# Kernel tuning notes

Hardware: AMD Instinct MI355X
Metric: run time of the kernel (lower is better)

## Reference

```python
import jax, jax.numpy as jnp
import numpy as np

HEADS = 8
DIM_HEAD = 64
SCALE = DIM_HEAD ** -0.5  # q scaling
EPS = 1e-5  # channel LayerNorm eps (float32)


def setup_inputs() -> dict:
    key = jax.random.key(0)
    ks = jax.random.split(key, 4)
    B, C, H, W = 8, 256, 64, 64
    hd = HEADS * DIM_HEAD  # 512
    x = jax.random.normal(ks[0], (B, C, H, W), dtype=jnp.float32)
    w_qkv = jax.random.normal(ks[1], (3 * hd, C), dtype=jnp.float32) * 0.02  # 1x1 conv, no bias
    w_out = jax.random.normal(ks[2], (C, hd), dtype=jnp.float32) * 0.02     # 1x1 conv
    b_out = jax.random.normal(ks[3], (C,), dtype=jnp.float32) * 0.02
    g_ln = jnp.ones((C,), dtype=jnp.float32)  # LayerNorm gamma
    return {"x": x, "w_qkv": w_qkv, "w_out": w_out, "b_out": b_out, "g_ln": g_ln}


def reference(x, w_qkv, w_out, b_out, g_ln):
    B, C, H, W = x.shape
    n = H * W
    hd = HEADS * DIM_HEAD
    # 1x1 conv == per-pixel matmul: [B,C,H,W] x [3hd,C] -> [B,3hd,H,W]
    qkv = jnp.einsum('bchw,oc->bohw', x, w_qkv).reshape(B, 3, HEADS, DIM_HEAD, n)
    q, k, v = qkv[:, 0], qkv[:, 1], qkv[:, 2]  # each [B,h,d,n]
    q = jax.nn.softmax(q, axis=-2) * SCALE      # softmax over head-dim d
    k = jax.nn.softmax(k, axis=-1)              # softmax over spatial n
    v = v / n
    context = jnp.einsum('bhdn,bhen->bhde', k, v)   # [B,h,d,e]
    out = jnp.einsum('bhde,bhdn->bhen', context, q)  # [B,h,e,n]
    out = out.reshape(B, hd, H, W)
    # to_out: 1x1 conv + bias, then channel-wise LayerNorm (gamma only)
    y = jnp.einsum('bchw,oc->bohw', out, w_out) + b_out[None, :, None, None]
    mean = jnp.mean(y, axis=1, keepdims=True)
    var = jnp.var(y, axis=1, keepdims=True)  # unbiased=False
    return (y - mean) * jax.lax.rsqrt(var + EPS) * g_ln[None, :, None, None]
```

## Files before the change

### kernel.cpp

```cpp
#include <hip/hip_runtime.h>
#include <stdint.h>


#define NB    8
#define CCH   256
#define NSP   4096
#define O3    1536
#define NH    8
#define DH    64
#define CSTR  136

typedef unsigned short u16;
typedef unsigned int   u32;
typedef __bf16 bf16;
typedef bf16  bf16x8 __attribute__((ext_vector_type(8)));
typedef float f32x4  __attribute__((ext_vector_type(4)));
typedef u16   u16x8  __attribute__((ext_vector_type(8)));
typedef u16   u16x4  __attribute__((ext_vector_type(4)));

__device__ __forceinline__ float b2f(u16 h) {
  union { u32 u; float f; } x; x.u = ((u32)h) << 16; return x.f;
}
__device__ __forceinline__ u16 f2b(float f) {
  union { float f; u32 u; } x; x.f = f;
  u32 r = x.u + 0x7fffu + ((x.u >> 16) & 1u);
  return (u16)(r >> 16);
}
__device__ __forceinline__ int detect_bf(const void* g) {
  return ((const u32*)g)[0] != 0x3F800000u;
}
__device__ __forceinline__ void ldg2lds16(const u16* g, u16* l) {
  __builtin_amdgcn_global_load_lds((const __attribute__((address_space(1))) void*)g,
                                   (__attribute__((address_space(3))) void*)l,
                                   16, 0, 0);
}

#define TSTR 68
__global__ __launch_bounds__(256) void k_prep(const void* __restrict__ xv,
                                              const void* __restrict__ wv,
                                              u16* __restrict__ xT,
                                              u16* __restrict__ Wb,
                                              float* __restrict__ S,
                                              const void* __restrict__ g_lnv) {
  const int isbf = detect_bf(g_lnv);
  const int t = threadIdx.x;
  if (blockIdx.z == 8) {
    const int tid = blockIdx.y * 64 + blockIdx.x;
    if (tid < 192) {
      const int idx = tid * 256 + t;
      const int row = idx >> 5, cu = idx & 31;
      int nr;
      if (row < 512)       nr = row;
      else if (row < 1024) nr = 512 + ((row - 512) >> 6) * 128 + (row & 63);
      else                 nr = 512 + ((row - 1024) >> 6) * 128 + 64 + (row & 63);
      const int didx = nr * 32 + cu;
      if (isbf) {
        reinterpret_cast<uint4*>(Wb)[didx] = reinterpret_cast<const uint4*>(wv)[idx];
      } else {
        float4 a = reinterpret_cast<const float4*>(wv)[idx * 2];
        float4 b = reinterpret_cast<const float4*>(wv)[idx * 2 + 1];
        ushort4 o0, o1;
        o0.x = f2b(a.x); o0.y = f2b(a.y); o0.z = f2b(a.z); o0.w = f2b(a.w);
        o1.x = f2b(b.x); o1.y = f2b(b.y); o1.z = f2b(b.z); o1.w = f2b(b.w);
        reinterpret_cast<ushort4*>(Wb)[didx * 2]     = o0;
        reinterpret_cast<ushort4*>(Wb)[didx * 2 + 1] = o1;
      }
    } else if (tid < 200) {
      reinterpret_cast<float2*>(S)[(tid - 192) * 256 + t] = (float2){0.f, 0.f};
    }
    return;
  }
  const int b = blockIdx.z, cb = blockIdx.y * 64, nb = blockIdx.x * 64;
  __shared__ u16 tile[64 * TSTR];
  if (isbf) {
    const u16* xb = (const u16*)xv;
#pragma unroll
    for (int rr = 0; rr < 2; ++rr) {
      const int u = t + 256 * rr;
      const int c = u >> 3, ch = u & 7;
      u16x8 v = *reinterpret_cast<const u16x8*>(
          xb + ((size_t)(b * CCH + cb + c) * NSP + nb + ch * 8));
      u16* dst = tile + c * TSTR + ch * 8;
      *reinterpret_cast<u16x4*>(dst)     = (u16x4){v[0], v[1], v[2], v[3]};
      *reinterpret_cast<u16x4*>(dst + 4) = (u16x4){v[4], v[5], v[6], v[7]};
    }
  } else {
    const float* xb = (const float*)xv;
#pragma unroll
    for (int rr = 0; rr < 4; ++rr) {
      const int u = t + 256 * rr;
      const int c = u >> 4, c4 = u & 15;
      float4 f = *reinterpret_cast<const float4*>(
          xb + ((size_t)(b * CCH + cb + c) * NSP + nb + c4 * 4));
      u16x4 o; o[0] = f2b(f.x); o[1] = f2b(f.y); o[2] = f2b(f.z); o[3] = f2b(f.w);
      *reinterpret_cast<u16x4*>(tile + c * TSTR + c4 * 4) = o;
    }
  }
  __syncthreads();
#pragma unroll
  for (int rr = 0; rr < 2; ++rr) {
    const int u = t + 256 * rr;
    const int n = u >> 3, cc = u & 7;
    u16x8 o;
#pragma unroll
    for (int e = 0; e < 8; ++e) o[e] = tile[(cc * 8 + e) * TSTR + n];
    *reinterpret_cast<u16x8*>(
        xT + ((size_t)(b * NSP + nb + n) * CCH + cb + cc * 8)) = o;
  }
}

__global__ __launch_bounds__(256) void k_q_mfma(const u16* __restrict__ Wb,
                                                const u16* __restrict__ xT,
                                                u16* __restrict__ qT) {
  __shared__ __align__(16) u16 As[4096];
  __shared__ __align__(16) u16 Bs[4096];
  const int b = blockIdx.z, m0 = blockIdx.y * 128, n0 = blockIdx.x * 128;
  const int t = threadIdx.x, w = t >> 6, l = t & 63;
  const int wm = (w >> 1) * 64, wn = (w & 1) * 64;
  const int fr = l & 15, quad = l >> 4;

  f32x4 acc[4][4];
#pragma unroll
  for (int i = 0; i < 4; ++i)
#pragma unroll
    for (int j = 0; j < 4; ++j) acc[i][j] = (f32x4){0.f, 0.f, 0.f, 0.f};

  {
    const u16* A = Wb;
    const u16* B = xT + (size_t)b * NSP * CCH;
    const int s0 = w * 2, s1 = s0 + 1;
    const int ra0 = s0 * 16 + (l >> 2);
    const int ra1 = s1 * 16 + (l >> 2);
    const int kc  = (l & 3) * 8;
    const int fq  = quad * 8;
    for (int k0 = 0; k0 < 256; k0 += 32) {
      ldg2lds16(A + (size_t)(m0 + ra0) * 256 + k0 + kc, As + s0 * 512);
      ldg2lds16(A + (size_t)(m0 + ra1) * 256 + k0 + kc, As + s1 * 512);
      ldg2lds16(B + (size_t)(n0 + ra0) * 256 + k0 + kc, Bs + s0 * 512);
      ldg2lds16(B + (size_t)(n0 + ra1) * 256 + k0 + kc, Bs + s1 * 512);
      asm volatile("s_waitcnt vmcnt(0)" ::: "memory");
      __syncthreads();
      bf16x8 af[4], bg[4];
#pragma unroll
      for (int i = 0; i < 4; ++i)
        af[i] = *reinterpret_cast<const bf16x8*>(As + (wm + i * 16 + fr) * 32 + fq);
#pragma unroll
      for (int j = 0; j < 4; ++j)
        bg[j] = *reinterpret_cast<const bf16x8*>(Bs + (wn + j * 16 + fr) * 32 + fq);
#pragma unroll
      for (int i = 0; i < 4; ++i)
#pragma unroll
        for (int j = 0; j < 4; ++j)
          acc[i][j] = __builtin_amdgcn_mfma_f32_16x16x32_bf16(af[i], bg[j], acc[i][j], 0, 0, 0);
      __syncthreads();
    }
  }

  const int h = (m0 >> 6) + (w >> 1);
  u16* qTb = qT + (size_t)b * NSP * 512 + h * 64;
#pragma unroll
  for (int j = 0; j < 4; ++j) {
    float s = 0.f;
#pragma unroll
    for (int i = 0; i < 4; ++i)
#pragma unroll
      for (int r = 0; r < 4; ++r) { acc[i][j][r] = __expf(acc[i][j][r]); s += acc[i][j][r]; }
    s += __shfl_xor(s, 16);
    s += __shfl_xor(s, 32);
    const float inv = 0.125f / s;
    const int n = n0 + wn + j * 16 + fr;
#pragma unroll
    for (int i = 0; i < 4; ++i) {
      ushort4 o;
      o.x = f2b(acc[i][j][0] * inv); o.y = f2b(acc[i][j][1] * inv);
      o.z = f2b(acc[i][j][2] * inv); o.w = f2b(acc[i][j][3] * inv);
      *reinterpret_cast<ushort4*>(qTb + (size_t)n * 512 + i * 16 + quad * 4) = o;
    }
  }
}

__global__ __launch_bounds__(256) void k_kv_mfma(const u16* __restrict__ Wb,
                                                 const u16* __restrict__ xT,
                                                 float* __restrict__ S,
                                                 float* __restrict__ ctxp) {
  __shared__ __align__(16) u16 pool[64 * CSTR * 2];
  u16* As = pool;
  u16* Bs = pool + 4096;
  u16* ekS = pool;
  u16* vS  = pool + 64 * CSTR;

  const int b = blockIdx.z, h = blockIdx.y, n0 = blockIdx.x * 128;
  const int m0 = 512 + h * 128;
  const int t = threadIdx.x, w = t >> 6, l = t & 63;
  const int wm = (w >> 1) * 64, wn = (w & 1) * 64;
  const int fr = l & 15, quad = l >> 4;

  f32x4 acc[4][4];
#pragma unroll
  for (int i = 0; i < 4; ++i)
#pragma unroll
    for (int j = 0; j < 4; ++j) acc[i][j] = (f32x4){0.f, 0.f, 0.f, 0.f};

  {
    const u16* A = Wb;
    const u16* B = xT + (size_t)b * NSP * CCH;
    const int s0 = w * 2, s1 = s0 + 1;
    const int ra0 = s0 * 16 + (l >> 2);
    const int ra1 = s1 * 16 + (l >> 2);
    const int kc  = (l & 3) * 8;
    const int fq  = quad * 8;
    for (int k0 = 0; k0 < 256; k0 += 32) {
      ldg2lds16(A + (size_t)(m0 + ra0) * 256 + k0 + kc, As + s0 * 512);
      ldg2lds16(A + (size_t)(m0 + ra1) * 256 + k0 + kc, As + s1 * 512);
      ldg2lds16(B + (size_t)(n0 + ra0) * 256 + k0 + kc, Bs + s0 * 512);
      ldg2lds16(B + (size_t)(n0 + ra1) * 256 + k0 + kc, Bs + s1 * 512);
      asm volatile("s_waitcnt vmcnt(0)" ::: "memory");
      __syncthreads();
      bf16x8 af[4], bg[4];
#pragma unroll
      for (int i = 0; i < 4; ++i)
        af[i] = *reinterpret_cast<const bf16x8*>(As + (wm + i * 16 + fr) * 32 + fq);
#pragma unroll
      for (int j = 0; j < 4; ++j)
        bg[j] = *reinterpret_cast<const bf16x8*>(Bs + (wn + j * 16 + fr) * 32 + fq);
#pragma unroll
      for (int i = 0; i < 4; ++i)
#pragma unroll
        for (int j = 0; j < 4; ++j)
          acc[i][j] = __builtin_amdgcn_mfma_f32_16x16x32_bf16(af[i], bg[j], acc[i][j], 0, 0, 0);
      __syncthreads();
    }
  }

  {
    u16* dstT = (w < 2) ? ekS : vS;
#pragma unroll
    for (int i = 0; i < 4; ++i)
#pragma unroll
      for (int r = 0; r < 4; ++r) {
        const int row = i * 16 + quad * 4 + r;
#pragma unroll
        for (int j = 0; j < 4; ++j) {
          float v = acc[i][j][r];
          if (w < 2) v = __expf(v);
          dstT[row * CSTR + wn + j * 16 + fr] = f2b(v);
        }
      }
  }
  __syncthreads();

  {
    const int d = t >> 2, seg = t & 3;
    float s = 0.f;
    const u16* src = ekS + d * CSTR + seg * 32;
#pragma unroll
    for (int m = 0; m < 32; ++m) s += b2f(src[m]);
    s += __shfl_xor(s, 1);
    s += __shfl_xor(s, 2);
    if ((t & 3) == 0) atomicAdd(&S[b * 512 + h * 64 + d], s);
  }

  f32x4 c2[4];
#pragma unroll
  for (int j = 0; j < 4; ++j) c2[j] = (f32x4){0.f, 0.f, 0.f, 0.f};
#pragma unroll
  for (int k0 = 0; k0 < 128; k0 += 32) {
    bf16x8 af = *reinterpret_cast<const bf16x8*>(ekS + (w * 16 + fr) * CSTR + k0 + quad * 8);
#pragma unroll
    for (int j = 0; j < 4; ++j) {
      bf16x8 bg = *reinterpret_cast<const bf16x8*>(vS + (j * 16 + fr) * CSTR + k0 + quad * 8);
      c2[j] = __builtin_amdgcn_mfma_f32_16x16x32_bf16(af, bg, c2[j], 0, 0, 0);
    }
  }
  float* cb = ctxp + ((size_t)blockIdx.x * 64 + b * NH + h) * 4096;
#pragma unroll
  for (int j = 0; j < 4; ++j)
#pragma unroll
    for (int r = 0; r < 4; ++r)
      cb[(w * 16 + quad * 4 + r) * 64 + j * 16 + fr] = c2[j][r];
}

__global__ __launch_bounds__(256) void k_fold(const float* __restrict__ ctxp,
                                              const void* __restrict__ w_outv,
                                              const float* __restrict__ S,
                                              u16* __restrict__ Mb,
                                              const void* __restrict__ g_lnv) {
  const int isbf = detect_bf(g_lnv);
  const int h = blockIdx.x, b = blockIdx.y, ds = blockIdx.z * 16;
  const int t = threadIdx.x;
  __shared__ float ctxS[16][64];
  __shared__ float invS[16];
  if (t < 16) invS[t] = (1.0f / 4096.0f) / S[b * 512 + h * 64 + ds + t];
  const size_t bhoff = (size_t)(b * NH + h) * 4096 + (size_t)ds * 64;
#pragma unroll
  for (int i = 0; i < 4; ++i) {
    const int idx = t + 256 * i;
    float s = 0.f;
#pragma unroll
    for (int ch = 0; ch < 32; ++ch)
      s += ctxp[(size_t)ch * 64 * 4096 + bhoff + idx];
    ctxS[idx >> 6][idx & 63] = s;
  }
  float wrow[64];
  if (isbf) {
    const u16* wsrc = (const u16*)w_outv + (size_t)t * 512 + h * DH;
#pragma unroll
    for (int e4 = 0; e4 < 64; e4 += 4) {
      ushort4 u = *reinterpret_cast<const ushort4*>(wsrc + e4);
      wrow[e4 + 0] = b2f(u.x); wrow[e4 + 1] = b2f(u.y);
      wrow[e4 + 2] = b2f(u.z); wrow[e4 + 3] = b2f(u.w);
    }
  } else {
    const float* wsrc = (const float*)w_outv + (size_t)t * 512 + h * DH;
#pragma unroll
    for (int e4 = 0; e4 < 64; e4 += 4) {
      float4 f = *reinterpret_cast<const float4*>(wsrc + e4);
      wrow[e4 + 0] = f.x; wrow[e4 + 1] = f.y;
      wrow[e4 + 2] = f.z; wrow[e4 + 3] = f.w;
    }
  }
  __syncthreads();
  u16* dst = Mb + ((size_t)(b * CCH + t)) * 512 + h * DH + ds;
  for (int d = 0; d < 16; ++d) {
    float s = 0.f;
#pragma unroll
    for (int e = 0; e < 64; e += 4) {
      float4 c4 = *reinterpret_cast<const float4*>(&ctxS[d][e]);
      s += wrow[e] * c4.x + wrow[e + 1] * c4.y + wrow[e + 2] * c4.z + wrow[e + 3] * c4.w;
    }
    dst[d] = f2b(s * invS[d]);
  }
}

__global__ __launch_bounds__(512) void k_mq_ln(const u16* __restrict__ Mb,
                                               const u16* __restrict__ qT,
                                               const void* __restrict__ b_outv,
                                               const void* __restrict__ g_lnv,
                                               void* __restrict__ outv) {
  __shared__ __align__(16) u16 As[256 * 32];
  __shared__ __align__(16) u16 Bs[64 * 32];
  __shared__ float redS[8][4][16];
  __shared__ float redQ[8][4][16];
  __shared__ float gS[256], bS[256];

  const int isbf = detect_bf(g_lnv);
  const int b  = blockIdx.y;
  const int n0 = blockIdx.x * 64;
  const int t  = threadIdx.x, w = t >> 6, l = t & 63;

  if (t < 256) {
    gS[t] = isbf ? b2f(((const u16*)g_lnv)[t]) : ((const float*)g_lnv)[t];
    bS[t] = isbf ? b2f(((const u16*)b_outv)[t]) : ((const float*)b_outv)[t];
  }

  f32x4 acc[2][4];
#pragma unroll
  for (int i = 0; i < 2; ++i)
#pragma unroll
    for (int j = 0; j < 4; ++j) acc[i][j] = (f32x4){0.f, 0.f, 0.f, 0.f};

  const u16* A = Mb + (size_t)b * CCH * 512;
  const u16* B = qT + (size_t)b * NSP * 512;
  const int lr = l >> 2, kc = (l & 3) * 8;
  const int fr = l & 15, fq = (l >> 4) * 8;
  const int quad = l >> 4;

  for (int k0 = 0; k0 < 512; k0 += 32) {
    ldg2lds16(A + (size_t)(w * 32 + lr) * 512 + k0 + kc, As + (2 * w) * 512);
    ldg2lds16(A + (size_t)(w * 32 + 16 + lr) * 512 + k0 + kc, As + (2 * w + 1) * 512);
    if (w < 4)
      ldg2lds16(B + (size_t)(n0 + w * 16 + lr) * 512 + k0 + kc, Bs + w * 512);
    asm volatile("s_waitcnt vmcnt(0)" ::: "memory");
    __syncthreads();
    bf16x8 af[2], bg[4];
#pragma unroll
    for (int i = 0; i < 2; ++i)
      af[i] = *reinterpret_cast<const bf16x8*>(As + (w * 32 + i * 16 + fr) * 32 + fq);
#pragma unroll
    for (int j = 0; j < 4; ++j)
      bg[j] = *reinterpret_cast<const bf16x8*>(Bs + (j * 16 + fr) * 32 + fq);
#pragma unroll
    for (int i = 0; i < 2; ++i)
#pragma unroll
      for (int j = 0; j < 4; ++j)
        acc[i][j] = __builtin_amdgcn_mfma_f32_16x16x32_bf16(af[i], bg[j], acc[i][j], 0, 0, 0);
    __syncthreads();
  }

  float ps[4] = {}, pq[4] = {};
#pragma unroll
  for (int i = 0; i < 2; ++i)
#pragma unroll
    for (int r = 0; r < 4; ++r) {
      const int c = w * 32 + i * 16 + quad * 4 + r;
      const float bi = bS[c];
#pragma unroll
      for (int j = 0; j < 4; ++j) {
        acc[i][j][r] += bi;
        ps[j] += acc[i][j][r];
        pq[j] += acc[i][j][r] * acc[i][j][r];
      }
    }
#pragma unroll
  for (int j = 0; j < 4; ++j) {
    ps[j] += __shfl_xor(ps[j], 16); ps[j] += __shfl_xor(ps[j], 32);
    pq[j] += __shfl_xor(pq[j], 16); pq[j] += __shfl_xor(pq[j], 32);
  }
  if (quad == 0) {
#pragma unroll
    for (int j = 0; j < 4; ++j) { redS[w][j][fr] = ps[j]; redQ[w][j][fr] = pq[j]; }
  }
  __syncthreads();
  float mean[4], inv[4];
#pragma unroll
  for (int j = 0; j < 4; ++j) {
    float s = 0.f, q = 0.f;
#pragma unroll
    for (int g = 0; g < 8; ++g) { s += redS[g][j][fr]; q += redQ[g][j][fr]; }
    const float mn = s * (1.0f / 256.0f);
    const float vr = q * (1.0f / 256.0f) - mn * mn;
    mean[j] = mn;
    inv[j] = rsqrtf(vr + 1e-5f);
  }

#pragma unroll
  for (int i = 0; i < 2; ++i)
#pragma unroll
    for (int r = 0; r < 4; ++r) {
      const int c = w * 32 + i * 16 + quad * 4 + r;
      const float g = gS[c];
#pragma unroll
      for (int j = 0; j < 4; ++j) {
        const int col = n0 + j * 16 + fr;
        const float o = (acc[i][j][r] - mean[j]) * inv[j] * g;
        const size_t idx = ((size_t)b * CCH + c) * NSP + col;
        if (isbf) ((u16*)outv)[idx] = f2b(o);
        else      ((float*)outv)[idx] = o;
      }
    }
}

extern "C" void kernel_launch(void* const* d_in, const int* in_sizes, int n_in,
                              void* d_out, int out_size, void* d_ws, size_t ws_size,
                              hipStream_t stream) {
  (void)in_sizes; (void)n_in; (void)out_size; (void)ws_size;
  const void* x     = d_in[0];
  const void* w_qkv = d_in[1];
  const void* w_out = d_in[2];
  const void* b_out = d_in[3];
  const void* g_ln  = d_in[4];

  char* ws = (char*)d_ws;
  u16*   Wb   = (u16*)(ws + 256);
  float* S    = (float*)(ws + 851968);
  u16*   xT   = (u16*)(ws + 1048576);
  u16*   qT   = (u16*)(ws + 17825792);
  float* ctxp = (float*)(ws + 51380224);
  u16*   Mb   = (u16*)(ws + 84934656);

  k_prep    <<<dim3(64, 4, 9),  256, 0, stream>>>(x, w_qkv, xT, Wb, S, g_ln);
  k_q_mfma  <<<dim3(32, 4, NB), 256, 0, stream>>>(Wb, xT, qT);
  k_kv_mfma <<<dim3(32, NH, NB),256, 0, stream>>>(Wb, xT, S, ctxp);
  k_fold    <<<dim3(NH, NB, 4), 256, 0, stream>>>(ctxp, w_out, S, Mb, g_ln);
  k_mq_ln   <<<dim3(64, NB),    512, 0, stream>>>(Mb, qT, b_out, g_ln, d_out);
}
```

Before: 173.5 us.

## Fuse q projection and softmax into final output GEMM via LDS

Removes the separate q-projection kernel and the global qT buffer. The final kernel now computes the q tile for its 64 pixels, applies the head-dim softmax, and stores it in a swizzled 64 KB LDS buffer, then runs the M·q GEMM reading q from LDS. The operands for both GEMMs are loaded straight from global into registers with no LDS staging or per-step barriers. This avoids a roughly 32 MB qT write and read-back plus one launch, but it cuts occupancy because of the large LDS footprint and relies on cache hits for the direct global loads.

```diff
diff --git a/kernel.cpp b/kernel.cpp
--- a/kernel.cpp
+++ b/kernel.cpp
@@ -109,12 +109,18 @@
   }
 }
 
-__global__ __launch_bounds__(256) void k_q_mfma(const u16* __restrict__ Wb,
-                                                const u16* __restrict__ xT,
-                                                u16* __restrict__ qT) {
-  __shared__ __align__(16) u16 As[4096];
-  __shared__ __align__(16) u16 Bs[4096];
-  const int b = blockIdx.z, m0 = blockIdx.y * 128, n0 = blockIdx.x * 128;
+__global__ __launch_bounds__(256) void k_kv_mfma(const u16* __restrict__ Wb,
+                                                 const u16* __restrict__ xT,
+                                                 float* __restrict__ S,
+                                                 float* __restrict__ ctxp) {
+  __shared__ __align__(16) u16 pool[64 * CSTR * 2];
+  u16* As = pool;
+  u16* Bs = pool + 4096;
+  u16* ekS = pool;
+  u16* vS  = pool + 64 * CSTR;
+
+  const int b = blockIdx.z, h = blockIdx.y, n0 = blockIdx.x * 128;
+  const int m0 = 512 + h * 128;
   const int t = threadIdx.x, w = t >> 6, l = t & 63;
   const int wm = (w >> 1) * 64, wn = (w & 1) * 64;
   const int fr = l & 15, quad = l >> 4;
@@ -156,82 +162,6 @@
     }
   }
 
-  const int h = (m0 >> 6) + (w >> 1);
-  u16* qTb = qT + (size_t)b * NSP * 512 + h * 64;
-#pragma unroll
-  for (int j = 0; j < 4; ++j) {
-    float s = 0.f;
-#pragma unroll
-    for (int i = 0; i < 4; ++i)
-#pragma unroll
-      for (int r = 0; r < 4; ++r) { acc[i][j][r] = __expf(acc[i][j][r]); s += acc[i][j][r]; }
-    s += __shfl_xor(s, 16);
-    s += __shfl_xor(s, 32);
-    const float inv = 0.125f / s;
-    const int n = n0 + wn + j * 16 + fr;
-#pragma unroll
-    for (int i = 0; i < 4; ++i) {
-      ushort4 o;
-      o.x = f2b(acc[i][j][0] * inv); o.y = f2b(acc[i][j][1] * inv);
-      o.z = f2b(acc[i][j][2] * inv); o.w = f2b(acc[i][j][3] * inv);
-      *reinterpret_cast<ushort4*>(qTb + (size_t)n * 512 + i * 16 + quad * 4) = o;
-    }
-  }
-}
-
-__global__ __launch_bounds__(256) void k_kv_mfma(const u16* __restrict__ Wb,
-                                                 const u16* __restrict__ xT,
-                                                 float* __restrict__ S,
-                                                 float* __restrict__ ctxp) {
-  __shared__ __align__(16) u16 pool[64 * CSTR * 2];
-  u16* As = pool;
-  u16* Bs = pool + 4096;
-  u16* ekS = pool;
-  u16* vS  = pool + 64 * CSTR;
-
-  const int b = blockIdx.z, h = blockIdx.y, n0 = blockIdx.x * 128;
-  const int m0 = 512 + h * 128;
-  const int t = threadIdx.x, w = t >> 6, l = t & 63;
-  const int wm = (w >> 1) * 64, wn = (w & 1) * 64;
-  const int fr = l & 15, quad = l >> 4;
-
-  f32x4 acc[4][4];
-#pragma unroll
-  for (int i = 0; i < 4; ++i)
-#pragma unroll
-    for (int j = 0; j < 4; ++j) acc[i][j] = (f32x4){0.f, 0.f, 0.f, 0.f};
-
-  {
-    const u16* A = Wb;
-    const u16* B = xT + (size_t)b * NSP * CCH;
-    const int s0 = w * 2, s1 = s0 + 1;
-    const int ra0 = s0 * 16 + (l >> 2);
-    const int ra1 = s1 * 16 + (l >> 2);
-    const int kc  = (l & 3) * 8;
-    const int fq  = quad * 8;
-    for (int k0 = 0; k0 < 256; k0 += 32) {
-      ldg2lds16(A + (size_t)(m0 + ra0) * 256 + k0 + kc, As + s0 * 512);
-      ldg2lds16(A + (size_t)(m0 + ra1) * 256 + k0 + kc, As + s1 * 512);
-      ldg2lds16(B + (size_t)(n0 + ra0) * 256 + k0 + kc, Bs + s0 * 512);
-      ldg2lds16(B + (size_t)(n0 + ra1) * 256 + k0 + kc, Bs + s1 * 512);
-      asm volatile("s_waitcnt vmcnt(0)" ::: "memory");
-      __syncthreads();
-      bf16x8 af[4], bg[4];
-#pragma unroll
-      for (int i = 0; i < 4; ++i)
-        af[i] = *reinterpret_cast<const bf16x8*>(As + (wm + i * 16 + fr) * 32 + fq);
-#pragma unroll
-      for (int j = 0; j < 4; ++j)
-        bg[j] = *reinterpret_cast<const bf16x8*>(Bs + (wn + j * 16 + fr) * 32 + fq);
-#pragma unroll
-      for (int i = 0; i < 4; ++i)
-#pragma unroll
-        for (int j = 0; j < 4; ++j)
-          acc[i][j] = __builtin_amdgcn_mfma_f32_16x16x32_bf16(af[i], bg[j], acc[i][j], 0, 0, 0);
-      __syncthreads();
-    }
-  }
-
   {
     u16* dstT = (w < 2) ? ekS : vS;
 #pragma unroll
@@ -332,13 +262,13 @@
   }
 }
 
-__global__ __launch_bounds__(512) void k_mq_ln(const u16* __restrict__ Mb,
-                                               const u16* __restrict__ qT,
-                                               const void* __restrict__ b_outv,
-                                               const void* __restrict__ g_lnv,
-                                               void* __restrict__ outv) {
-  __shared__ __align__(16) u16 As[256 * 32];
-  __shared__ __align__(16) u16 Bs[64 * 32];
+__global__ __launch_bounds__(512) void k_qmq_ln(const u16* __restrict__ Wb,
+                                                const u16* __restrict__ xT,
+                                                const u16* __restrict__ Mb,
+                                                const void* __restrict__ b_outv,
+                                                const void* __restrict__ g_lnv,
+                                                void* __restrict__ outv) {
+  __shared__ __align__(16) u16 qS[64 * 512];
   __shared__ float redS[8][4][16];
   __shared__ float redQ[8][4][16];
   __shared__ float gS[256], bS[256];
@@ -347,44 +277,87 @@
   const int b  = blockIdx.y;
   const int n0 = blockIdx.x * 64;
   const int t  = threadIdx.x, w = t >> 6, l = t & 63;
+  const int fr = l & 15, quad = l >> 4;
 
   if (t < 256) {
     gS[t] = isbf ? b2f(((const u16*)g_lnv)[t]) : ((const float*)g_lnv)[t];
     bS[t] = isbf ? b2f(((const u16*)b_outv)[t]) : ((const float*)b_outv)[t];
   }
 
+  {
+    f32x4 qa[4][4];
+#pragma unroll
+    for (int i = 0; i < 4; ++i)
+#pragma unroll
+      for (int j = 0; j < 4; ++j) qa[i][j] = (f32x4){0.f, 0.f, 0.f, 0.f};
+
+    const u16* Aq = Wb + (size_t)(w * 64 + fr) * 256 + quad * 8;
+    const u16* Bx = xT + ((size_t)b * NSP + n0 + fr) * 256 + quad * 8;
+#pragma unroll
+    for (int k0 = 0; k0 < 256; k0 += 32) {
+      bf16x8 af[4], bg[4];
+#pragma unroll
+      for (int i = 0; i < 4; ++i)
+        af[i] = *reinterpret_cast<const bf16x8*>(Aq + (size_t)i * 16 * 256 + k0);
+#pragma unroll
+      for (int j = 0; j < 4; ++j)
+        bg[j] = *reinterpret_cast<const bf16x8*>(Bx + (size_t)j * 16 * 256 + k0);
+#pragma unroll
+      for (int i = 0; i < 4; ++i)
+#pragma unroll
+        for (int j = 0; j < 4; ++j)
+          qa[i][j] = __builtin_amdgcn_mfma_f32_16x16x32_bf16(af[i], bg[j], qa[i][j], 0, 0, 0);
+    }
+
+#pragma unroll
+    for (int j = 0; j < 4; ++j) {
+      float s = 0.f;
+#pragma unroll
+      for (int i = 0; i < 4; ++i)
+#pragma unroll
+        for (int r = 0; r < 4; ++r) { qa[i][j][r] = __expf(qa[i][j][r]); s += qa[i][j][r]; }
+      s += __shfl_xor(s, 16);
+      s += __shfl_xor(s, 32);
+      const float inv = 0.125f / s;
+      const int n   = j * 16 + fr;
+      const int swz = (n & 7) << 4;
+#pragma unroll
+      for (int i = 0; i < 4; ++i) {
+        ushort4 o;
+        o.x = f2b(qa[i][j][0] * inv); o.y = f2b(qa[i][j][1] * inv);
+        o.z = f2b(qa[i][j][2] * inv); o.w = f2b(qa[i][j][3] * inv);
+        const int hd2 = (w * 64 + i * 16 + quad * 4) * 2;
+        *reinterpret_cast<ushort4*>(
+            reinterpret_cast<char*>(qS) + ((n * 1024 + hd2) ^ swz)) = o;
+      }
+    }
+  }
+  __syncthreads();
+
   f32x4 acc[2][4];
 #pragma unroll
   for (int i = 0; i < 2; ++i)
 #pragma unroll
     for (int j = 0; j < 4; ++j) acc[i][j] = (f32x4){0.f, 0.f, 0.f, 0.f};
 
-  const u16* A = Mb + (size_t)b * CCH * 512;
-  const u16* B = qT + (size_t)b * NSP * 512;
-  const int lr = l >> 2, kc = (l & 3) * 8;
-  const int fr = l & 15, fq = (l >> 4) * 8;
-  const int quad = l >> 4;
-
+  const u16* Am = Mb + ((size_t)b * CCH + w * 32 + fr) * 512 + quad * 8;
+#pragma unroll 4
   for (int k0 = 0; k0 < 512; k0 += 32) {
-    ldg2lds16(A + (size_t)(w * 32 + lr) * 512 + k0 + kc, As + (2 * w) * 512);
-    ldg2lds16(A + (size_t)(w * 32 + 16 + lr) * 512 + k0 + kc, As + (2 * w + 1) * 512);
-    if (w < 4)
-      ldg2lds16(B + (size_t)(n0 + w * 16 + lr) * 512 + k0 + kc, Bs + w * 512);
-    asm volatile("s_waitcnt vmcnt(0)" ::: "memory");
-    __syncthreads();
     bf16x8 af[2], bg[4];
-#pragma unroll
-    for (int i = 0; i < 2; ++i)
-      af[i] = *reinterpret_cast<const bf16x8*>(As + (w * 32 + i * 16 + fr) * 32 + fq);
-#pragma unroll
-    for (int j = 0; j < 4; ++j)
-      bg[j] = *reinterpret_cast<const bf16x8*>(Bs + (j * 16 + fr) * 32 + fq);
+    af[0] = *reinterpret_cast<const bf16x8*>(Am + k0);
+    af[1] = *reinterpret_cast<const bf16x8*>(Am + 16 * 512 + k0);
+#pragma unroll
+    for (int j = 0; j < 4; ++j) {
+      const int n = j * 16 + fr;
+      const int byteoff = (n * 1024 + k0 * 2 + quad * 16) ^ ((n & 7) << 4);
+      bg[j] = *reinterpret_cast<const bf16x8*>(
+          reinterpret_cast<const char*>(qS) + byteoff);
+    }
 #pragma unroll
     for (int i = 0; i < 2; ++i)
 #pragma unroll
       for (int j = 0; j < 4; ++j)
         acc[i][j] = __builtin_amdgcn_mfma_f32_16x16x32_bf16(af[i], bg[j], acc[i][j], 0, 0, 0);
-    __syncthreads();
   }
 
   float ps[4] = {}, pq[4] = {};
@@ -454,13 +427,11 @@
   u16*   Wb   = (u16*)(ws + 256);
   float* S    = (float*)(ws + 851968);
   u16*   xT   = (u16*)(ws + 1048576);
-  u16*   qT   = (u16*)(ws + 17825792);
-  float* ctxp = (float*)(ws + 51380224);
-  u16*   Mb   = (u16*)(ws + 84934656);
+  float* ctxp = (float*)(ws + 17825792);
+  u16*   Mb   = (u16*)(ws + 51380224);
 
   k_prep    <<<dim3(64, 4, 9),  256, 0, stream>>>(x, w_qkv, xT, Wb, S, g_ln);
-  k_q_mfma  <<<dim3(32, 4, NB), 256, 0, stream>>>(Wb, xT, qT);
   k_kv_mfma <<<dim3(32, NH, NB),256, 0, stream>>>(Wb, xT, S, ctxp);
   k_fold    <<<dim3(NH, NB, 4), 256, 0, stream>>>(ctxp, w_out, S, Mb, g_ln);
-  k_mq_ln   <<<dim3(64, NB),    512, 0, stream>>>(Mb, qT, b_out, g_ln, d_out);
-}
+  k_qmq_ln  <<<dim3(64, NB),    512, 0, stream>>>(Wb, xT, Mb, b_out, g_ln, d_out);
+}
```

Measured after the change: 188.4 us. 1.09x slower.
